# Optimization experiments

Hardware: AMD Instinct MI355X
Metric: run time of the kernel (lower is better)

Reference implementation:

```python
import jax, jax.numpy as jnp
import numpy as np

B_SZ, L, H, P = 16, 1024, 256, 256
DT_MIN, DT_MAX = 1e-3, 1e-1


def setup_inputs() -> dict:
    key = jax.random.key(0)
    ks = jax.random.split(key, 6)
    u = jax.random.normal(ks[0], (B_SZ, L, H), dtype=jnp.float32)
    # Stable diagonal init (stands in for HiPPO-LegS diag: negative real part,
    # spread imaginary parts) so exp(Lambda*Delta) has |.|<1 over long scans.
    Lambda_re = -0.5 * jnp.ones((P,), jnp.float32)
    Lambda_im = jnp.pi * jnp.arange(P, dtype=jnp.float32)
    Bp = jax.random.normal(ks[1], (P, H, 2), jnp.float32) / jnp.sqrt(2.0 * H)  # (P,H,2) real/imag
    Cp = jax.random.normal(ks[2], (H, P, 2), jnp.float32) / jnp.sqrt(2.0 * P)  # (H,P,2) real/imag
    D = jax.random.normal(ks[3], (H,), jnp.float32)
    log_step = (jax.random.uniform(ks[4], (P, 1), jnp.float32)
                * (jnp.log(DT_MAX) - jnp.log(DT_MIN)) + jnp.log(DT_MIN))
    return {"u": u, "Lambda_re": Lambda_re, "Lambda_im": Lambda_im,
            "B": Bp, "C": Cp, "D": D, "log_step": log_step}


def _binop(ei, ej):
    # S5 associative scan element: (A, Bu); compose linear recurrences.
    ai, bi = ei
    aj, bj = ej
    return aj * ai, aj * bi + bj


def reference(u, Lambda_re, Lambda_im, B, C, D, log_step):
    # clip_eigs=False, step_rescale=1.0, conj_sym=True, discretization='zoh'
    Lambda = Lambda_re + 1j * Lambda_im                     # (P,) complex
    B_tilde = B[..., 0] + 1j * B[..., 1]                    # (P,H) complex
    C_tilde = C[..., 0] + 1j * C[..., 1]                    # (H,P) complex
    Delta = jnp.exp(log_step[:, 0])                         # (P,)
    # ZOH discretization
    Lambda_bar = jnp.exp(Lambda * Delta)                    # (P,)
    B_bar = ((Lambda_bar - 1.0) / Lambda)[:, None] * B_tilde  # (P,H)
    # Input projection: (B, L, P) complex
    Bu = jnp.einsum('ph,blh->blp', B_bar, u.astype(B_bar.dtype))
    Lam = jnp.broadcast_to(Lambda_bar, Bu.shape)            # (B, L, P)
    # Parallel associative scan over time axis
    _, xs = jax.lax.associative_scan(_binop, (Lam, Bu), axis=1)  # states (B,L,P)
    # Output projection; conj_sym -> 2 * real part
    ys = 2.0 * jnp.einsum('hp,blp->blh', C_tilde, xs).real  # (B,L,H)
    return ys + D * u                                       # feedthrough
```

## Files before the change

### kernel.cpp

```cpp
#include <hip/hip_runtime.h>
#include <hip/hip_bf16.h>
#include <math.h>

#define BB     16
#define LSEQ   1024
#define HH     256
#define PP     256
#define LC     32
#define NC     (LSEQ/LC)
#define NCHUNK (BB*NC)

#define OFF_W1T  0u
#define OFF_W2T  262144u
#define OFF_PW   524288u
#define OFF_CEND 655360u
#define OFF_BAR  2752512u

typedef __attribute__((ext_vector_type(8))) short short8;
typedef __attribute__((ext_vector_type(4))) float floatx4;
typedef unsigned long long ull;

__device__ __forceinline__ float bf2f(unsigned hs) {
    union { unsigned u; float f; } v; v.u = hs << 16; return v.f;
}
__device__ __forceinline__ unsigned short f2bs(float f) {
    __hip_bfloat16 h = __float2bfloat16(f);
    union { __hip_bfloat16 h; unsigned short s; } v; v.h = h; return v.s;
}
__device__ __forceinline__ unsigned packbf(float r, float i) {
    return (unsigned)f2bs(r) | ((unsigned)f2bs(i) << 16);
}
__device__ __forceinline__ void async16(const void* g, void* l) {
    __builtin_amdgcn_global_load_lds(
        (const __attribute__((address_space(1))) unsigned*)g,
        (__attribute__((address_space(3))) unsigned*)l, 16, 0, 0);
}
__device__ __forceinline__ float2 lam_pow(float lr, float li, float dtt) {
    float m = expf(lr * dtt);
    return make_float2(m * cosf(li * dtt), m * sinf(li * dtt));
}
__device__ __forceinline__ void cohst64(ull* p, float2 v) {
    ull b; __builtin_memcpy(&b, &v, 8);
    __hip_atomic_store(p, b, __ATOMIC_RELAXED, __HIP_MEMORY_SCOPE_AGENT);
}

__device__ __forceinline__ void batchbar(char* base) {
    asm volatile("s_waitcnt vmcnt(0)" ::: "memory");
    __syncthreads();
    if (threadIdx.x == 0) {
        const unsigned b = blockIdx.x >> 5;
        unsigned* cnt  = (unsigned*)(base + b * 64);
        unsigned* flag = (unsigned*)(base + 2048 + b * 64);
        if (__hip_atomic_fetch_add(cnt, 1u, __ATOMIC_RELAXED,
                                   __HIP_MEMORY_SCOPE_AGENT) == 31u) {
            __hip_atomic_store(flag, 1u, __ATOMIC_RELAXED, __HIP_MEMORY_SCOPE_AGENT);
        } else {
            for (int it = 0; it < (1 << 18); ++it) {
                if (__hip_atomic_load(flag, __ATOMIC_RELAXED, __HIP_MEMORY_SCOPE_AGENT))
                    break;
                __builtin_amdgcn_s_sleep(2);
            }
        }
    }
    __syncthreads();
}

__global__ void k_prep(const float* __restrict__ Bm, const float* __restrict__ Cm,
                       const float* __restrict__ Lr, const float* __restrict__ Li,
                       const float* __restrict__ ls, char* __restrict__ ws) {
    int blk = blockIdx.x, t = threadIdx.x;
    if (blk < 256) {
        if (t < 128) {
            int p = blk;
            float lr = Lr[p], li = Li[p];
            float dt = expf(ls[p]);
            float2 lam = lam_pow(lr, li, dt);
            float den = lr * lr + li * li;
            float nr = lam.x - 1.0f, ni = lam.y;
            float cr = (nr * lr + ni * li) / den;
            float ci = (ni * lr - nr * li) / den;
            float4 bv = *(const float4*)(Bm + (size_t)p * 512 + 4 * t);
            unsigned* w1u = (unsigned*)(ws + OFF_W1T);
            w1u[(2 * p) * 128 + t]     = packbf(cr * bv.x - ci * bv.y, cr * bv.z - ci * bv.w);
            w1u[(2 * p + 1) * 128 + t] = packbf(cr * bv.y + ci * bv.x, cr * bv.w + ci * bv.z);
            if (t <= 32)
                ((float2*)(ws + OFF_PW))[t * 256 + p] = lam_pow(lr, li, dt * (float)t);
        }
        if (blk == 0)
            ((float4*)(ws + OFF_BAR))[t] = make_float4(0.f, 0.f, 0.f, 0.f);
    } else {
        int h = blk - 256, p = t;
        float c_r = Cm[(h * PP + p) * 2 + 0];
        float c_i = Cm[(h * PP + p) * 2 + 1];
        ((unsigned*)(ws + OFF_W2T))[h * 256 + p] = packbf(2.0f * c_r, -2.0f * c_i);
    }
}

#define XSTRS 520
#define XSTRD 260
#define CARR_OFF 33280
#define B1_OFF  16384
#define B2_OFF  35328

__global__ __launch_bounds__(512, 4) void k_main(
        const float* __restrict__ u, const float* __restrict__ Lr,
        const float* __restrict__ Li, const float* __restrict__ ls,
        const float* __restrict__ D, float* __restrict__ out,
        char* __restrict__ ws) {
    extern __shared__ char smem[];
    const int tid = threadIdx.x, bc = blockIdx.x;
    const int wave = tid >> 6, lane = tid & 63;
    const int q = lane >> 4, rr = lane & 15;
    const int m0 = bc * LC;
    const int fs = (lane >> 3) & 3;
    const int fr = (rr >> 1) & 3;

    const char* W1 = (const char*)(ws + OFF_W1T);
    {
        char* dst = smem + B1_OFF + wave * 4096;
        #pragma unroll
        for (int i = 0; i < 4; ++i) {
            int n = i * 64 + lane;
            int R = wave * 64 + (n >> 2);
            async16(W1 + (size_t)R * 512 + (((n & 3) ^ fs) << 4), dst + n * 16);
        }
    }

    const int arow = tid >> 4, acol = (tid & 15) * 16;
    {
        float4 uv[4];
        const float* up = u + (size_t)(m0 + arow) * 256 + acol;
        #pragma unroll
        for (int i = 0; i < 4; ++i) uv[i] = *(const float4*)(up + 4 * i);
        unsigned pk[8];
        #pragma unroll
        for (int i = 0; i < 4; ++i) {
            pk[2 * i]     = packbf(uv[i].x, uv[i].y);
            pk[2 * i + 1] = packbf(uv[i].z, uv[i].w);
        }
        const int kb = acol * 2;
        const int msk = (arow & 7) << 4;
        char* A = smem;
        *(uint4*)(A + arow * 512 + (kb ^ msk))        = make_uint4(pk[0], pk[1], pk[2], pk[3]);
        *(uint4*)(A + arow * 512 + ((kb + 16) ^ msk)) = make_uint4(pk[4], pk[5], pk[6], pk[7]);
    }

    {
        char* dst = smem + B1_OFF + 32768 + wave * 4096;
        const char* src = W1 + 64;
        #pragma unroll
        for (int i = 0; i < 4; ++i) {
            int n = i * 64 + lane;
            int R = wave * 64 + (n >> 2);
            async16(src + (size_t)R * 512 + (((n & 3) ^ fs) << 4), dst + n * 16);
        }
    }
    __syncthreads();

    {
        const char* A = smem;
        const int amask = (rr & 7) << 4;
        floatx4 acc[2][4];
        #pragma unroll
        for (int i = 0; i < 2; ++i)
            #pragma unroll
            for (int j = 0; j < 4; ++j) acc[i][j] = (floatx4)0.0f;

        #pragma unroll
        for (int t = 0; t < 8; ++t) {
            if (t < 7) { asm volatile("s_waitcnt vmcnt(4)" ::: "memory"); }
            else       { asm volatile("s_waitcnt vmcnt(0)" ::: "memory"); }
            const char* bb = smem + B1_OFF + (t & 1) * 32768 + wave * 4096;
            const int kbA = t * 64 + q * 16;
            short8 a0 = *(const short8*)(A + rr * 512 + (kbA ^ amask));
            short8 a1 = *(const short8*)(A + (16 + rr) * 512 + (kbA ^ amask));
            short8 bfr[4];
            #pragma unroll
            for (int j = 0; j < 4; ++j)
                bfr[j] = *(const short8*)(bb + (j * 16 + rr) * 64 + ((q ^ fr) << 4));
            asm volatile("s_waitcnt lgkmcnt(0)" ::: "memory");
            __builtin_amdgcn_sched_barrier(0);
            if (t < 6) {
                char* dst = smem + B1_OFF + (t & 1) * 32768 + wave * 4096;
                const char* src = W1 + (t + 2) * 64;
                #pragma unroll
                for (int i = 0; i < 4; ++i) {
                    int n = i * 64 + lane;
                    int R = wave * 64 + (n >> 2);
                    async16(src + (size_t)R * 512 + (((n & 3) ^ fs) << 4), dst + n * 16);
                }
            }
            #pragma unroll
            for (int j = 0; j < 4; ++j) {
                acc[0][j] = __builtin_amdgcn_mfma_f32_16x16x32_bf16(a0, bfr[j], acc[0][j], 0, 0, 0);
                acc[1][j] = __builtin_amdgcn_mfma_f32_16x16x32_bf16(a1, bfr[j], acc[1][j], 0, 0, 0);
            }
        }
        __syncthreads();
        unsigned short* X = (unsigned short*)smem;
        #pragma unroll
        for (int i = 0; i < 2; ++i)
            #pragma unroll
            for (int j = 0; j < 4; ++j)
                #pragma unroll
                for (int r0 = 0; r0 < 4; ++r0)
                    X[(i * 16 + q * 4 + r0) * XSTRS + wave * 64 + j * 16 + rr] =
                        f2bs(acc[i][j][r0]);
        __syncthreads();
    }

    if (tid < 256) {
        const int pq = tid;
        const float2 lam = lam_pow(Lr[pq], Li[pq], expf(ls[pq]));
        unsigned* X32 = (unsigned*)smem;
        float xr = 0.0f, xi = 0.0f;
        #pragma unroll
        for (int j = 0; j < LC; ++j) {
            unsigned cv = X32[j * XSTRD + pq];
            float br = bf2f(cv & 0xffffu), bi = bf2f(cv >> 16);
            float nr = fmaf(lam.x, xr, fmaf(-lam.y, xi, br));
            float ni = fmaf(lam.x, xi, fmaf(lam.y, xr, bi));
            xr = nr; xi = ni;
            X32[j * XSTRD + pq] = packbf(xr, xi);
        }
        cohst64((ull*)(ws + OFF_CEND) + (size_t)bc * 256 + pq, make_float2(xr, xi));
    } else {
        const char* W2 = (const char*)(ws + OFF_W2T);
        char* B2 = smem + B2_OFF;
        const int t4 = tid - 256;
        const int f0 = (t4 >> 3) & 3;
        #pragma unroll
        for (int pan = 0; pan < 2; ++pan) {
            #pragma unroll
            for (int i = 0; i < 4; ++i) {
                int c = i * 256 + t4;
                int R = c >> 2;
                async16(W2 + (size_t)R * 1024 + pan * 64 + (((c & 3) ^ f0) << 4),
                        B2 + pan * 16384 + c * 16);
            }
        }
    }
    batchbar(ws + OFF_BAR);

    {
        float2* carrs = (float2*)(smem + CARR_OFF);
        if (tid < 256) {
            const int p = tid;
            const int c = bc & (NC - 1);
            const int b0 = bc & ~(NC - 1);
            const float2* cend = (const float2*)(ws + OFF_CEND);
            const float2 g = lam_pow(Lr[p], Li[p], expf(ls[p]) * (float)LC);
            float sr = 0.0f, si = 0.0f;
            float gpr = 1.0f, gpi = 0.0f;
            #pragma unroll
            for (int k = 0; k < NC - 1; ++k) {
                int idx = c - 1 - k; idx = idx < 0 ? 0 : idx;
                float2 e = cend[(size_t)(b0 + idx) * 256 + p];
                float er = (k < c) ? e.x : 0.0f;
                float ei = (k < c) ? e.y : 0.0f;
                sr = fmaf(gpr, er, fmaf(-gpi, ei, sr));
                si = fmaf(gpr, ei, fmaf(gpi, er, si));
                float t2 = gpr * g.x - gpi * g.y;
                gpi = gpr * g.y + gpi * g.x; gpr = t2;
            }
            carrs[p] = make_float2(sr, si);
        }
        __syncthreads();
    }

    {
        float2* carrs = (float2*)(smem + CARR_OFF);
        unsigned* X32 = (unsigned*)smem;
        const float2* pw = (const float2*)(ws + OFF_PW);
        const int frow = tid >> 4, fcol = tid & 15;
        const float2* pwr = pw + (size_t)(frow + 1) * 256;
        #pragma unroll 4
        for (int e = 0; e < 16; ++e) {
            int p = fcol + e * 16;
            unsigned cv = X32[frow * XSTRD + p];
            float2 pwv = pwr[p];
            float2 cav = carrs[p];
            float fr2 = pwv.x * cav.x - pwv.y * cav.y;
            float fi2 = pwv.x * cav.y + pwv.y * cav.x;
            X32[frow * XSTRD + p] =
                packbf(bf2f(cv & 0xffffu) + fr2, bf2f(cv >> 16) + fi2);
        }
        __syncthreads();
    }

    {
        const char* W2 = (const char*)(ws + OFF_W2T);
        const char* Xb = (const char*)smem;
        floatx4 acc[2][2];
        #pragma unroll
        for (int i = 0; i < 2; ++i)
            #pragma unroll
            for (int j = 0; j < 2; ++j) acc[i][j] = (floatx4)0.0f;

        #pragma unroll
        for (int t = 0; t < 16; ++t) {
            if (t < 15) { asm volatile("s_waitcnt vmcnt(2)" ::: "memory"); }
            else        { asm volatile("s_waitcnt vmcnt(0)" ::: "memory"); }
            const char* bbuf = smem + B2_OFF + (t & 1) * 16384 + wave * 2048;
            const int kbA = t * 64 + q * 16;
            short8 a0 = *(const short8*)(Xb + rr * (XSTRS * 2) + kbA);
            short8 a1 = *(const short8*)(Xb + (16 + rr) * (XSTRS * 2) + kbA);
            short8 bfr[2];
            #pragma unroll
            for (int j = 0; j < 2; ++j)
                bfr[j] = *(const short8*)(bbuf + (j * 16 + rr) * 64 + ((q ^ fr) << 4));
            asm volatile("s_waitcnt lgkmcnt(0)" ::: "memory");
            __builtin_amdgcn_sched_barrier(0);
            if (t < 14) {
                char* dst = smem + B2_OFF + (t & 1) * 16384 + wave * 2048;
                const char* src = W2 + (t + 2) * 64;
                #pragma unroll
                for (int i = 0; i < 2; ++i) {
                    int n = i * 64 + lane;
                    int R = wave * 32 + (n >> 2);
                    async16(src + (size_t)R * 1024 + (((n & 3) ^ fs) << 4), dst + n * 16);
                }
            }
            #pragma unroll
            for (int j = 0; j < 2; ++j) {
                acc[0][j] = __builtin_amdgcn_mfma_f32_16x16x32_bf16(a0, bfr[j], acc[0][j], 0, 0, 0);
                acc[1][j] = __builtin_amdgcn_mfma_f32_16x16x32_bf16(a1, bfr[j], acc[1][j], 0, 0, 0);
            }
        }

        #pragma unroll
        for (int i = 0; i < 2; ++i) {
            int mbase = m0 + i * 16 + q * 4;
            #pragma unroll
            for (int j = 0; j < 2; ++j) {
                int col = wave * 32 + j * 16 + rr;
                #pragma unroll
                for (int r0 = 0; r0 < 4; ++r0) {
                    int rw = mbase + r0;
                    size_t gi = (size_t)rw * 256 + col;
                    out[gi] = acc[i][j][r0] + D[col] * u[gi];
                }
            }
        }
    }
}

extern "C" void kernel_launch(void* const* d_in, const int* in_sizes, int n_in,
                              void* d_out, int out_size, void* d_ws, size_t ws_size,
                              hipStream_t stream) {
    const float* u  = (const float*)d_in[0];
    const float* Lr = (const float*)d_in[1];
    const float* Li = (const float*)d_in[2];
    const float* Bm = (const float*)d_in[3];
    const float* Cm = (const float*)d_in[4];
    const float* D  = (const float*)d_in[5];
    const float* ls = (const float*)d_in[6];
    float* out = (float*)d_out;
    char* ws = (char*)d_ws;

    k_prep<<<512, 256, 0, stream>>>(Bm, Cm, Lr, Li, ls, ws);
    k_main<<<NCHUNK, 512, 81920, stream>>>(u, Lr, Li, ls, D, out, ws);
}
```

Baseline: 104.1 us.

## Split fused scan kernel into two launches instead of a spin barrier

Replaces the software grid barrier (atomic counter plus flag spin) inside one kernel with two kernels. The first computes the input projection and chunk-local scans and writes per-step states to global workspace. The second computes carries, applies them and does the output projection. This removes reliance on co-residency and spin waits, but adds a kernel launch and a round trip of the full bf16 state tensor through global memory. The second kernel's shared-memory footprint also shrinks.

```diff
diff --git a/kernel.cpp b/kernel.cpp
--- a/kernel.cpp
+++ b/kernel.cpp
@@ -14,11 +14,10 @@
 #define OFF_W2T  262144u
 #define OFF_PW   524288u
 #define OFF_CEND 655360u
-#define OFF_BAR  2752512u
+#define OFF_XS   2752512u
 
 typedef __attribute__((ext_vector_type(8))) short short8;
 typedef __attribute__((ext_vector_type(4))) float floatx4;
-typedef unsigned long long ull;
 
 __device__ __forceinline__ float bf2f(unsigned hs) {
     union { unsigned u; float f; } v; v.u = hs << 16; return v.f;
@@ -38,31 +37,6 @@
 __device__ __forceinline__ float2 lam_pow(float lr, float li, float dtt) {
     float m = expf(lr * dtt);
     return make_float2(m * cosf(li * dtt), m * sinf(li * dtt));
-}
-__device__ __forceinline__ void cohst64(ull* p, float2 v) {
-    ull b; __builtin_memcpy(&b, &v, 8);
-    __hip_atomic_store(p, b, __ATOMIC_RELAXED, __HIP_MEMORY_SCOPE_AGENT);
-}
-
-__device__ __forceinline__ void batchbar(char* base) {
-    asm volatile("s_waitcnt vmcnt(0)" ::: "memory");
-    __syncthreads();
-    if (threadIdx.x == 0) {
-        const unsigned b = blockIdx.x >> 5;
-        unsigned* cnt  = (unsigned*)(base + b * 64);
-        unsigned* flag = (unsigned*)(base + 2048 + b * 64);
-        if (__hip_atomic_fetch_add(cnt, 1u, __ATOMIC_RELAXED,
-                                   __HIP_MEMORY_SCOPE_AGENT) == 31u) {
-            __hip_atomic_store(flag, 1u, __ATOMIC_RELAXED, __HIP_MEMORY_SCOPE_AGENT);
-        } else {
-            for (int it = 0; it < (1 << 18); ++it) {
-                if (__hip_atomic_load(flag, __ATOMIC_RELAXED, __HIP_MEMORY_SCOPE_AGENT))
-                    break;
-                __builtin_amdgcn_s_sleep(2);
-            }
-        }
-    }
-    __syncthreads();
 }
 
 __global__ void k_prep(const float* __restrict__ Bm, const float* __restrict__ Cm,
@@ -86,8 +60,6 @@
             if (t <= 32)
                 ((float2*)(ws + OFF_PW))[t * 256 + p] = lam_pow(lr, li, dt * (float)t);
         }
-        if (blk == 0)
-            ((float4*)(ws + OFF_BAR))[t] = make_float4(0.f, 0.f, 0.f, 0.f);
     } else {
         int h = blk - 256, p = t;
         float c_r = Cm[(h * PP + p) * 2 + 0];
@@ -102,10 +74,9 @@
 #define B1_OFF  16384
 #define B2_OFF  35328
 
-__global__ __launch_bounds__(512, 4) void k_main(
+__global__ __launch_bounds__(512, 4) void k_g1(
         const float* __restrict__ u, const float* __restrict__ Lr,
         const float* __restrict__ Li, const float* __restrict__ ls,
-        const float* __restrict__ D, float* __restrict__ out,
         char* __restrict__ ws) {
     extern __shared__ char smem[];
     const int tid = threadIdx.x, bc = blockIdx.x;
@@ -213,6 +184,7 @@
         const int pq = tid;
         const float2 lam = lam_pow(Lr[pq], Li[pq], expf(ls[pq]));
         unsigned* X32 = (unsigned*)smem;
+        unsigned* xs32 = (unsigned*)(ws + OFF_XS);
         float xr = 0.0f, xi = 0.0f;
         #pragma unroll
         for (int j = 0; j < LC; ++j) {
@@ -221,75 +193,98 @@
             float nr = fmaf(lam.x, xr, fmaf(-lam.y, xi, br));
             float ni = fmaf(lam.x, xi, fmaf(lam.y, xr, bi));
             xr = nr; xi = ni;
-            X32[j * XSTRD + pq] = packbf(xr, xi);
-        }
-        cohst64((ull*)(ws + OFF_CEND) + (size_t)bc * 256 + pq, make_float2(xr, xi));
-    } else {
-        const char* W2 = (const char*)(ws + OFF_W2T);
-        char* B2 = smem + B2_OFF;
-        const int t4 = tid - 256;
-        const int f0 = (t4 >> 3) & 3;
-        #pragma unroll
-        for (int pan = 0; pan < 2; ++pan) {
-            #pragma unroll
-            for (int i = 0; i < 4; ++i) {
-                int c = i * 256 + t4;
+            xs32[(size_t)(m0 + j) * 256 + pq] = packbf(xr, xi);
+        }
+        ((float2*)(ws + OFF_CEND))[(size_t)bc * 256 + pq] = make_float2(xr, xi);
+    }
+}
+
+__global__ __launch_bounds__(512, 4) void k_g2(
+        const char* __restrict__ ws_c, const float* __restrict__ D,
+        const float* __restrict__ u, float* __restrict__ out,
+        const float* __restrict__ Lr, const float* __restrict__ Li,
+        const float* __restrict__ ls) {
+    extern __shared__ char smem[];
+    const int tid = threadIdx.x, bc = blockIdx.x;
+    const int wave = tid >> 6, lane = tid & 63;
+    const int q = lane >> 4, rr = lane & 15;
+    const int m0 = bc * LC;
+    const int fs = (lane >> 3) & 3;
+    const int fr = (rr >> 1) & 3;
+    const char* W2 = (const char*)(ws_c + OFF_W2T);
+    const unsigned* xs32 = (const unsigned*)(ws_c + OFF_XS);
+    char* B2 = smem + B2_OFF;
+
+    {
+        const int f0 = (tid >> 3) & 3;
+        #pragma unroll
+        for (int pan = 0; pan < 2; ++pan)
+            #pragma unroll
+            for (int i = 0; i < 2; ++i) {
+                int c = i * 512 + tid;
                 int R = c >> 2;
                 async16(W2 + (size_t)R * 1024 + pan * 64 + (((c & 3) ^ f0) << 4),
                         B2 + pan * 16384 + c * 16);
             }
-        }
-    }
-    batchbar(ws + OFF_BAR);
-
-    {
-        float2* carrs = (float2*)(smem + CARR_OFF);
-        if (tid < 256) {
-            const int p = tid;
-            const int c = bc & (NC - 1);
-            const int b0 = bc & ~(NC - 1);
-            const float2* cend = (const float2*)(ws + OFF_CEND);
-            const float2 g = lam_pow(Lr[p], Li[p], expf(ls[p]) * (float)LC);
-            float sr = 0.0f, si = 0.0f;
-            float gpr = 1.0f, gpi = 0.0f;
-            #pragma unroll
-            for (int k = 0; k < NC - 1; ++k) {
-                int idx = c - 1 - k; idx = idx < 0 ? 0 : idx;
-                float2 e = cend[(size_t)(b0 + idx) * 256 + p];
-                float er = (k < c) ? e.x : 0.0f;
-                float ei = (k < c) ? e.y : 0.0f;
-                sr = fmaf(gpr, er, fmaf(-gpi, ei, sr));
-                si = fmaf(gpr, ei, fmaf(gpi, er, si));
-                float t2 = gpr * g.x - gpi * g.y;
-                gpi = gpr * g.y + gpi * g.x; gpr = t2;
-            }
-            carrs[p] = make_float2(sr, si);
-        }
-        __syncthreads();
-    }
-
-    {
-        float2* carrs = (float2*)(smem + CARR_OFF);
+    }
+
+    const int row = tid >> 4, qd = tid & 15;
+    const int grow = m0 + row;
+    uint4 xv0 = *(const uint4*)(xs32 + (size_t)grow * 256 + qd * 16);
+    uint4 xv1 = *(const uint4*)(xs32 + (size_t)grow * 256 + qd * 16 + 4);
+    uint4 xv2 = *(const uint4*)(xs32 + (size_t)grow * 256 + qd * 16 + 8);
+    uint4 xv3 = *(const uint4*)(xs32 + (size_t)grow * 256 + qd * 16 + 12);
+
+    float2* carrs = (float2*)(smem + CARR_OFF);
+    if (tid < 256) {
+        const int p = tid;
+        const int c = bc & (NC - 1);
+        const int b0 = bc & ~(NC - 1);
+        const float2* cend = (const float2*)(ws_c + OFF_CEND);
+        const float2 g = lam_pow(Lr[p], Li[p], expf(ls[p]) * (float)LC);
+        float sr = 0.0f, si = 0.0f;
+        float gpr = 1.0f, gpi = 0.0f;
+        #pragma unroll
+        for (int k = 0; k < NC - 1; ++k) {
+            int idx = c - 1 - k; idx = idx < 0 ? 0 : idx;
+            float2 e = cend[(size_t)(b0 + idx) * 256 + p];
+            float er = (k < c) ? e.x : 0.0f;
+            float ei = (k < c) ? e.y : 0.0f;
+            sr = fmaf(gpr, er, fmaf(-gpi, ei, sr));
+            si = fmaf(gpr, ei, fmaf(gpi, er, si));
+            float t2 = gpr * g.x - gpi * g.y;
+            gpi = gpr * g.y + gpi * g.x; gpr = t2;
+        }
+        carrs[p] = make_float2(sr, si);
+    }
+    __syncthreads();
+
+    {
         unsigned* X32 = (unsigned*)smem;
-        const float2* pw = (const float2*)(ws + OFF_PW);
-        const int frow = tid >> 4, fcol = tid & 15;
-        const float2* pwr = pw + (size_t)(frow + 1) * 256;
-        #pragma unroll 4
+        const float2* pw = (const float2*)(ws_c + OFF_PW);
+        const float2* pwr = pw + (size_t)(row + 1) * 256 + qd * 16;
+        const float2* cap = carrs + qd * 16;
+        unsigned xv[16] = {xv0.x, xv0.y, xv0.z, xv0.w, xv1.x, xv1.y, xv1.z, xv1.w,
+                           xv2.x, xv2.y, xv2.z, xv2.w, xv3.x, xv3.y, xv3.z, xv3.w};
+        unsigned o[16];
+        #pragma unroll
         for (int e = 0; e < 16; ++e) {
-            int p = fcol + e * 16;
-            unsigned cv = X32[frow * XSTRD + p];
-            float2 pwv = pwr[p];
-            float2 cav = carrs[p];
+            float2 pwv = pwr[e];
+            float2 cav = cap[e];
             float fr2 = pwv.x * cav.x - pwv.y * cav.y;
             float fi2 = pwv.x * cav.y + pwv.y * cav.x;
-            X32[frow * XSTRD + p] =
-                packbf(bf2f(cv & 0xffffu) + fr2, bf2f(cv >> 16) + fi2);
-        }
-        __syncthreads();
-    }
-
-    {
-        const char* W2 = (const char*)(ws + OFF_W2T);
+            o[e] = packbf(bf2f(xv[e] & 0xffffu) + fr2, bf2f(xv[e] >> 16) + fi2);
+        }
+        unsigned* dst = X32 + row * XSTRD + qd * 16;
+        *(uint4*)(dst)      = make_uint4(o[0], o[1], o[2], o[3]);
+        *(uint4*)(dst + 4)  = make_uint4(o[4], o[5], o[6], o[7]);
+        *(uint4*)(dst + 8)  = make_uint4(o[8], o[9], o[10], o[11]);
+        *(uint4*)(dst + 12) = make_uint4(o[12], o[13], o[14], o[15]);
+    }
+    asm volatile("s_waitcnt vmcnt(0)" ::: "memory");
+    __syncthreads();
+
+    {
         const char* Xb = (const char*)smem;
         floatx4 acc[2][2];
         #pragma unroll
@@ -359,5 +354,6 @@
     char* ws = (char*)d_ws;
 
     k_prep<<<512, 256, 0, stream>>>(Bm, Cm, Lr, Li, ls, ws);
-    k_main<<<NCHUNK, 512, 81920, stream>>>(u, Lr, Li, ls, D, out, ws);
-}
+    k_g1<<<NCHUNK, 512, 81920, stream>>>(u, Lr, Li, ls, ws);
+    k_g2<<<NCHUNK, 512, 68096, stream>>>(ws, D, u, out, Lr, Li, ls);
+}
```

Result: slower. 115.4 us (+10.9%).

## Process two time chunks per block with triple-buffered weight panels

Applied to the files above, without the earlier changes.

Each block now handles 64 rows (two 32-step chunks) instead of 32, halving the grid to 256 blocks and doubling MFMA tile reuse of the streamed B/C weight panels. The weight pipelines move from double to triple buffering, and the per-iteration lgkmcnt wait and sched barrier are dropped. The W2 prefetch is now issued by all threads before the scan, and both halves of the block run the scan. This costs more LDS (128KB) and lower occupancy (2 blocks per CU in the launch bounds). The per-batch barrier counts change to 16 blocks per batch.

```diff
diff --git a/kernel.cpp b/kernel.cpp
--- a/kernel.cpp
+++ b/kernel.cpp
@@ -8,7 +8,7 @@
 #define PP     256
 #define LC     32
 #define NC     (LSEQ/LC)
-#define NCHUNK (BB*NC)
+#define NBLK   256
 
 #define OFF_W1T  0u
 #define OFF_W2T  262144u
@@ -48,11 +48,11 @@
     asm volatile("s_waitcnt vmcnt(0)" ::: "memory");
     __syncthreads();
     if (threadIdx.x == 0) {
-        const unsigned b = blockIdx.x >> 5;
+        const unsigned b = blockIdx.x >> 4;
         unsigned* cnt  = (unsigned*)(base + b * 64);
         unsigned* flag = (unsigned*)(base + 2048 + b * 64);
         if (__hip_atomic_fetch_add(cnt, 1u, __ATOMIC_RELAXED,
-                                   __HIP_MEMORY_SCOPE_AGENT) == 31u) {
+                                   __HIP_MEMORY_SCOPE_AGENT) == 15u) {
             __hip_atomic_store(flag, 1u, __ATOMIC_RELAXED, __HIP_MEMORY_SCOPE_AGENT);
         } else {
             for (int it = 0; it < (1 << 18); ++it) {
@@ -98,11 +98,14 @@
 
 #define XSTRS 520
 #define XSTRD 260
-#define CARR_OFF 33280
-#define B1_OFF  16384
-#define B2_OFF  35328
-
-__global__ __launch_bounds__(512, 4) void k_main(
+#define B1_OFF   32768
+#define CARR_OFF 66560
+#define B2_OFF   70656
+#define LDS_SZ   131072
+
+#define MFMA16(a, b, c) __builtin_amdgcn_mfma_f32_16x16x32_bf16((a), (b), (c), 0, 0, 0)
+
+__global__ __launch_bounds__(512, 2) void k_main(
         const float* __restrict__ u, const float* __restrict__ Lr,
         const float* __restrict__ Li, const float* __restrict__ ls,
         const float* __restrict__ D, float* __restrict__ out,
@@ -111,43 +114,24 @@
     const int tid = threadIdx.x, bc = blockIdx.x;
     const int wave = tid >> 6, lane = tid & 63;
     const int q = lane >> 4, rr = lane & 15;
-    const int m0 = bc * LC;
+    const int m0 = bc * 64;
     const int fs = (lane >> 3) & 3;
     const int fr = (rr >> 1) & 3;
-
     const char* W1 = (const char*)(ws + OFF_W1T);
-    {
-        char* dst = smem + B1_OFF + wave * 4096;
-        #pragma unroll
-        for (int i = 0; i < 4; ++i) {
-            int n = i * 64 + lane;
-            int R = wave * 64 + (n >> 2);
-            async16(W1 + (size_t)R * 512 + (((n & 3) ^ fs) << 4), dst + n * 16);
-        }
-    }
-
-    const int arow = tid >> 4, acol = (tid & 15) * 16;
-    {
-        float4 uv[4];
+    const char* W2 = (const char*)(ws + OFF_W2T);
+
+    const int arow = tid >> 3, acol = (tid & 7) * 32;
+    float4 uv[8];
+    {
         const float* up = u + (size_t)(m0 + arow) * 256 + acol;
         #pragma unroll
-        for (int i = 0; i < 4; ++i) uv[i] = *(const float4*)(up + 4 * i);
-        unsigned pk[8];
-        #pragma unroll
-        for (int i = 0; i < 4; ++i) {
-            pk[2 * i]     = packbf(uv[i].x, uv[i].y);
-            pk[2 * i + 1] = packbf(uv[i].z, uv[i].w);
-        }
-        const int kb = acol * 2;
-        const int msk = (arow & 7) << 4;
-        char* A = smem;
-        *(uint4*)(A + arow * 512 + (kb ^ msk))        = make_uint4(pk[0], pk[1], pk[2], pk[3]);
-        *(uint4*)(A + arow * 512 + ((kb + 16) ^ msk)) = make_uint4(pk[4], pk[5], pk[6], pk[7]);
-    }
-
-    {
-        char* dst = smem + B1_OFF + 32768 + wave * 4096;
-        const char* src = W1 + 64;
+        for (int i = 0; i < 8; ++i) uv[i] = *(const float4*)(up + 4 * i);
+    }
+
+    #pragma unroll
+    for (int pan = 0; pan < 2; ++pan) {
+        char* dst = smem + B1_OFF + pan * 32768 + wave * 4096;
+        const char* src = W1 + pan * 64;
         #pragma unroll
         for (int i = 0; i < 4; ++i) {
             int n = i * 64 + lane;
@@ -155,14 +139,30 @@
             async16(src + (size_t)R * 512 + (((n & 3) ^ fs) << 4), dst + n * 16);
         }
     }
+
+    {
+        unsigned pk[16];
+        #pragma unroll
+        for (int i = 0; i < 8; ++i) {
+            pk[2 * i]     = packbf(uv[i].x, uv[i].y);
+            pk[2 * i + 1] = packbf(uv[i].z, uv[i].w);
+        }
+        const int kb = acol * 2;
+        const int msk = (arow & 7) << 4;
+        char* A = smem;
+        #pragma unroll
+        for (int s = 0; s < 4; ++s)
+            *(uint4*)(A + arow * 512 + ((kb + 16 * s) ^ msk)) =
+                make_uint4(pk[4 * s], pk[4 * s + 1], pk[4 * s + 2], pk[4 * s + 3]);
+    }
     __syncthreads();
 
     {
         const char* A = smem;
         const int amask = (rr & 7) << 4;
-        floatx4 acc[2][4];
-        #pragma unroll
-        for (int i = 0; i < 2; ++i)
+        floatx4 acc[4][4];
+        #pragma unroll
+        for (int i = 0; i < 4; ++i)
             #pragma unroll
             for (int j = 0; j < 4; ++j) acc[i][j] = (floatx4)0.0f;
 
@@ -170,18 +170,8 @@
         for (int t = 0; t < 8; ++t) {
             if (t < 7) { asm volatile("s_waitcnt vmcnt(4)" ::: "memory"); }
             else       { asm volatile("s_waitcnt vmcnt(0)" ::: "memory"); }
-            const char* bb = smem + B1_OFF + (t & 1) * 32768 + wave * 4096;
-            const int kbA = t * 64 + q * 16;
-            short8 a0 = *(const short8*)(A + rr * 512 + (kbA ^ amask));
-            short8 a1 = *(const short8*)(A + (16 + rr) * 512 + (kbA ^ amask));
-            short8 bfr[4];
-            #pragma unroll
-            for (int j = 0; j < 4; ++j)
-                bfr[j] = *(const short8*)(bb + (j * 16 + rr) * 64 + ((q ^ fr) << 4));
-            asm volatile("s_waitcnt lgkmcnt(0)" ::: "memory");
-            __builtin_amdgcn_sched_barrier(0);
             if (t < 6) {
-                char* dst = smem + B1_OFF + (t & 1) * 32768 + wave * 4096;
+                char* dst = smem + B1_OFF + ((t + 2) % 3) * 32768 + wave * 4096;
                 const char* src = W1 + (t + 2) * 64;
                 #pragma unroll
                 for (int i = 0; i < 4; ++i) {
@@ -190,16 +180,25 @@
                     async16(src + (size_t)R * 512 + (((n & 3) ^ fs) << 4), dst + n * 16);
                 }
             }
-            #pragma unroll
-            for (int j = 0; j < 4; ++j) {
-                acc[0][j] = __builtin_amdgcn_mfma_f32_16x16x32_bf16(a0, bfr[j], acc[0][j], 0, 0, 0);
-                acc[1][j] = __builtin_amdgcn_mfma_f32_16x16x32_bf16(a1, bfr[j], acc[1][j], 0, 0, 0);
-            }
+            const char* bb = smem + B1_OFF + (t % 3) * 32768 + wave * 4096;
+            const int kbA = t * 64 + q * 16;
+            short8 a[4], bfr[4];
+            #pragma unroll
+            for (int i = 0; i < 4; ++i)
+                a[i] = *(const short8*)(A + (i * 16 + rr) * 512 + (kbA ^ amask));
+            #pragma unroll
+            for (int j = 0; j < 4; ++j)
+                bfr[j] = *(const short8*)(bb + (j * 16 + rr) * 64 + ((q ^ fr) << 4));
+            #pragma unroll
+            for (int i = 0; i < 4; ++i)
+                #pragma unroll
+                for (int j = 0; j < 4; ++j)
+                    acc[i][j] = MFMA16(a[i], bfr[j], acc[i][j]);
         }
         __syncthreads();
         unsigned short* X = (unsigned short*)smem;
         #pragma unroll
-        for (int i = 0; i < 2; ++i)
+        for (int i = 0; i < 4; ++i)
             #pragma unroll
             for (int j = 0; j < 4; ++j)
                 #pragma unroll
@@ -209,77 +208,76 @@
         __syncthreads();
     }
 
-    if (tid < 256) {
-        const int pq = tid;
+    {
+        char* B2 = smem + B2_OFF;
+        const int f0 = (tid >> 3) & 3;
+        #pragma unroll
+        for (int pan = 0; pan < 2; ++pan)
+            #pragma unroll
+            for (int i = 0; i < 2; ++i) {
+                int c = i * 512 + tid;
+                int R = c >> 2;
+                async16(W2 + (size_t)R * 1024 + pan * 64 + (((c & 3) ^ f0) << 4),
+                        B2 + pan * 16384 + c * 16);
+            }
+    }
+
+    {
+        const int hf = tid >> 8, pq = tid & 255;
+        const int cc = 2 * bc + hf;
         const float2 lam = lam_pow(Lr[pq], Li[pq], expf(ls[pq]));
         unsigned* X32 = (unsigned*)smem;
         float xr = 0.0f, xi = 0.0f;
         #pragma unroll
         for (int j = 0; j < LC; ++j) {
-            unsigned cv = X32[j * XSTRD + pq];
+            unsigned cv = X32[(hf * 32 + j) * XSTRD + pq];
             float br = bf2f(cv & 0xffffu), bi = bf2f(cv >> 16);
             float nr = fmaf(lam.x, xr, fmaf(-lam.y, xi, br));
             float ni = fmaf(lam.x, xi, fmaf(lam.y, xr, bi));
             xr = nr; xi = ni;
-            X32[j * XSTRD + pq] = packbf(xr, xi);
-        }
-        cohst64((ull*)(ws + OFF_CEND) + (size_t)bc * 256 + pq, make_float2(xr, xi));
-    } else {
-        const char* W2 = (const char*)(ws + OFF_W2T);
-        char* B2 = smem + B2_OFF;
-        const int t4 = tid - 256;
-        const int f0 = (t4 >> 3) & 3;
-        #pragma unroll
-        for (int pan = 0; pan < 2; ++pan) {
-            #pragma unroll
-            for (int i = 0; i < 4; ++i) {
-                int c = i * 256 + t4;
-                int R = c >> 2;
-                async16(W2 + (size_t)R * 1024 + pan * 64 + (((c & 3) ^ f0) << 4),
-                        B2 + pan * 16384 + c * 16);
-            }
-        }
+            X32[(hf * 32 + j) * XSTRD + pq] = packbf(xr, xi);
+        }
+        cohst64((ull*)(ws + OFF_CEND) + (size_t)cc * 256 + pq, make_float2(xr, xi));
     }
     batchbar(ws + OFF_BAR);
 
     {
         float2* carrs = (float2*)(smem + CARR_OFF);
-        if (tid < 256) {
-            const int p = tid;
-            const int c = bc & (NC - 1);
-            const int b0 = bc & ~(NC - 1);
-            const float2* cend = (const float2*)(ws + OFF_CEND);
-            const float2 g = lam_pow(Lr[p], Li[p], expf(ls[p]) * (float)LC);
-            float sr = 0.0f, si = 0.0f;
-            float gpr = 1.0f, gpi = 0.0f;
-            #pragma unroll
-            for (int k = 0; k < NC - 1; ++k) {
-                int idx = c - 1 - k; idx = idx < 0 ? 0 : idx;
-                float2 e = cend[(size_t)(b0 + idx) * 256 + p];
-                float er = (k < c) ? e.x : 0.0f;
-                float ei = (k < c) ? e.y : 0.0f;
-                sr = fmaf(gpr, er, fmaf(-gpi, ei, sr));
-                si = fmaf(gpr, ei, fmaf(gpi, er, si));
-                float t2 = gpr * g.x - gpi * g.y;
-                gpi = gpr * g.y + gpi * g.x; gpr = t2;
-            }
-            carrs[p] = make_float2(sr, si);
-        }
+        const int hf = tid >> 8, p = tid & 255;
+        const int c = ((bc & 15) << 1) | hf;
+        const int b0 = (bc >> 4) << 5;
+        const float2* cend = (const float2*)(ws + OFF_CEND);
+        const float2 g = lam_pow(Lr[p], Li[p], expf(ls[p]) * (float)LC);
+        float sr = 0.0f, si = 0.0f;
+        float gpr = 1.0f, gpi = 0.0f;
+        #pragma unroll
+        for (int k = 0; k < NC - 1; ++k) {
+            int idx = c - 1 - k; idx = idx < 0 ? 0 : idx;
+            float2 e = cend[(size_t)(b0 + idx) * 256 + p];
+            float er = (k < c) ? e.x : 0.0f;
+            float ei = (k < c) ? e.y : 0.0f;
+            sr = fmaf(gpr, er, fmaf(-gpi, ei, sr));
+            si = fmaf(gpr, ei, fmaf(gpi, er, si));
+            float t2 = gpr * g.x - gpi * g.y;
+            gpi = gpr * g.y + gpi * g.x; gpr = t2;
+        }
+        carrs[hf * 256 + p] = make_float2(sr, si);
         __syncthreads();
     }
 
     {
-        float2* carrs = (float2*)(smem + CARR_OFF);
+        const float2* carrs = (const float2*)(smem + CARR_OFF);
         unsigned* X32 = (unsigned*)smem;
         const float2* pw = (const float2*)(ws + OFF_PW);
-        const int frow = tid >> 4, fcol = tid & 15;
-        const float2* pwr = pw + (size_t)(frow + 1) * 256;
-        #pragma unroll 4
-        for (int e = 0; e < 16; ++e) {
-            int p = fcol + e * 16;
+        const int frow = tid >> 3, f8 = tid & 7;
+        const float2* pwr = pw + (size_t)((frow & 31) + 1) * 256;
+        const float2* cap = carrs + (frow >> 5) * 256;
+        #pragma unroll 8
+        for (int e = 0; e < 32; ++e) {
+            int p = f8 + e * 8;
             unsigned cv = X32[frow * XSTRD + p];
             float2 pwv = pwr[p];
-            float2 cav = carrs[p];
+            float2 cav = cap[p];
             float fr2 = pwv.x * cav.x - pwv.y * cav.y;
             float fi2 = pwv.x * cav.y + pwv.y * cav.x;
             X32[frow * XSTRD + p] =
@@ -289,11 +287,10 @@
     }
 
     {
-        const char* W2 = (const char*)(ws + OFF_W2T);
         const char* Xb = (const char*)smem;
-        floatx4 acc[2][2];
-        #pragma unroll
-        for (int i = 0; i < 2; ++i)
+        floatx4 acc[4][2];
+        #pragma unroll
+        for (int i = 0; i < 4; ++i)
             #pragma unroll
             for (int j = 0; j < 2; ++j) acc[i][j] = (floatx4)0.0f;
 
@@ -301,18 +298,8 @@
         for (int t = 0; t < 16; ++t) {
             if (t < 15) { asm volatile("s_waitcnt vmcnt(2)" ::: "memory"); }
             else        { asm volatile("s_waitcnt vmcnt(0)" ::: "memory"); }
-            const char* bbuf = smem + B2_OFF + (t & 1) * 16384 + wave * 2048;
-            const int kbA = t * 64 + q * 16;
-            short8 a0 = *(const short8*)(Xb + rr * (XSTRS * 2) + kbA);
-            short8 a1 = *(const short8*)(Xb + (16 + rr) * (XSTRS * 2) + kbA);
-            short8 bfr[2];
-            #pragma unroll
-            for (int j = 0; j < 2; ++j)
-                bfr[j] = *(const short8*)(bbuf + (j * 16 + rr) * 64 + ((q ^ fr) << 4));
-            asm volatile("s_waitcnt lgkmcnt(0)" ::: "memory");
-            __builtin_amdgcn_sched_barrier(0);
             if (t < 14) {
-                char* dst = smem + B2_OFF + (t & 1) * 16384 + wave * 2048;
+                char* dst = smem + B2_OFF + ((t + 2) % 3) * 16384 + wave * 2048;
                 const char* src = W2 + (t + 2) * 64;
                 #pragma unroll
                 for (int i = 0; i < 2; ++i) {
@@ -321,15 +308,24 @@
                     async16(src + (size_t)R * 1024 + (((n & 3) ^ fs) << 4), dst + n * 16);
                 }
             }
-            #pragma unroll
-            for (int j = 0; j < 2; ++j) {
-                acc[0][j] = __builtin_amdgcn_mfma_f32_16x16x32_bf16(a0, bfr[j], acc[0][j], 0, 0, 0);
-                acc[1][j] = __builtin_amdgcn_mfma_f32_16x16x32_bf16(a1, bfr[j], acc[1][j], 0, 0, 0);
-            }
-        }
-
-        #pragma unroll
-        for (int i = 0; i < 2; ++i) {
+            const char* bbuf = smem + B2_OFF + (t % 3) * 16384 + wave * 2048;
+            const int kbA = t * 64 + q * 16;
+            short8 a[4], bfr[2];
+            #pragma unroll
+            for (int i = 0; i < 4; ++i)
+                a[i] = *(const short8*)(Xb + (i * 16 + rr) * (XSTRS * 2) + kbA);
+            #pragma unroll
+            for (int j = 0; j < 2; ++j)
+                bfr[j] = *(const short8*)(bbuf + (j * 16 + rr) * 64 + ((q ^ fr) << 4));
+            #pragma unroll
+            for (int i = 0; i < 4; ++i)
+                #pragma unroll
+                for (int j = 0; j < 2; ++j)
+                    acc[i][j] = MFMA16(a[i], bfr[j], acc[i][j]);
+        }
+
+        #pragma unroll
+        for (int i = 0; i < 4; ++i) {
             int mbase = m0 + i * 16 + q * 4;
             #pragma unroll
             for (int j = 0; j < 2; ++j) {
@@ -359,5 +355,5 @@
     char* ws = (char*)d_ws;
 
     k_prep<<<512, 256, 0, stream>>>(Bm, Cm, Lr, Li, ls, ws);
-    k_main<<<NCHUNK, 512, 81920, stream>>>(u, Lr, Li, ls, D, out, ws);
-}
+    k_main<<<NBLK, 512, LDS_SZ, stream>>>(u, Lr, Li, ls, D, out, ws);
+}
```

After: 101.7 us. -2.3%, faster.
